# Kernel optimization log

Hardware: AMD Instinct MI355X
Metric: run time of the kernel (lower is better)

## Reference

```python
import jax, jax.numpy as jnp
import numpy as np

C_M, C_Z, C_H = 256, 128, 32
EPS = 1e-3
LN_EPS = 1e-5


def setup_inputs() -> dict:
    key = jax.random.key(0)
    ks = jax.random.split(key, 10)
    S, R = 128, 256
    inp = {
        'm_1': jax.random.normal(ks[0], (S, R, C_M), jnp.float32),
        'm_2': jax.random.normal(ks[1], (S, R, C_M), jnp.float32),
        'mask_1': jnp.ones((S, R), jnp.float32),
        'mask_2': jnp.ones((S, R), jnp.float32),
        # LayerNorm params
        'ln1_w': jnp.ones((C_M,), jnp.float32),
        'ln1_b': jnp.zeros((C_M,), jnp.float32),
        'ln2_w': jnp.ones((C_M,), jnp.float32),
        'ln2_b': jnp.zeros((C_M,), jnp.float32),
        # Linear params
        'w1': jax.random.normal(ks[2], (C_M, C_H), jnp.float32) * (1.0 / np.sqrt(C_M)),
        'b1': jnp.zeros((C_H,), jnp.float32),
        'w2': jax.random.normal(ks[3], (C_M, C_H), jnp.float32) * (1.0 / np.sqrt(C_M)),
        'b2': jnp.zeros((C_H,), jnp.float32),
        'w_out': jax.random.normal(ks[4], (C_H * C_H, C_Z), jnp.float32) * 0.02,
        'b_out': jnp.zeros((C_Z,), jnp.float32),
    }
    return inp


def _layer_norm(x, w, b):
    mu = jnp.mean(x, axis=-1, keepdims=True)
    var = jnp.mean(jnp.square(x - mu), axis=-1, keepdims=True)
    return (x - mu) * jax.lax.rsqrt(var + LN_EPS) * w + b


def reference(m_1, m_2, mask_1, mask_2, ln1_w, ln1_b, ln2_w, ln2_b,
              w1, b1, w2, b2, w_out, b_out):
    # m_*: [S, R, C_M]; mask_*: [S, R]
    a = (_layer_norm(m_1, ln1_w, ln1_b) @ w1 + b1) * mask_1[..., None]  # [S,R,H]
    b = (_layer_norm(m_2, ln2_w, ln2_b) @ w2 + b2) * mask_2[..., None]  # [S,R,H]
    # outer product mean over sequence dim: [R, R, H, H]
    outer = jnp.einsum('sic,sje->ijce', a, b)
    S, R, H = a.shape
    outer = outer.reshape(R, R, H * H)
    z = outer @ w_out + b_out  # [R, R, C_Z]
    norm = jnp.einsum('si,sj->ij', mask_1, mask_2)[..., None] + EPS  # [R,R,1]
    return z / norm
```

## Files before the change

kernel.cpp:

```cpp
#include <hip/hip_runtime.h>
#include <hip/hip_bf16.h>

#define S_DIM 128
#define R_DIM 256
#define CM    256
#define H_DIM 32
#define CZ    128

typedef short s8v   __attribute__((ext_vector_type(8)));
typedef float f32x4 __attribute__((ext_vector_type(4)));
typedef float f32x16 __attribute__((ext_vector_type(16)));
using bf16 = __hip_bfloat16;

static __device__ __forceinline__ unsigned short bf16_bits(float f) {
  return __builtin_bit_cast(unsigned short, __float2bfloat16(f));
}

static __device__ __forceinline__ void gload_lds16(const void* g, void* l) {
  __builtin_amdgcn_global_load_lds(
      (const __attribute__((address_space(1))) unsigned int*)g,
      (__attribute__((address_space(3))) unsigned int*)l, 16, 0, 0);
}

__global__ __launch_bounds__(256) void opm_prep(
    const float* __restrict__ w_out,
    const float* __restrict__ mask1, const float* __restrict__ mask2,
    const float* __restrict__ w1, const float* __restrict__ w2,
    bf16* __restrict__ wT2, float* __restrict__ rnorm, bf16* __restrict__ wF)
{
  const int b   = blockIdx.x;
  const int tid = threadIdx.x;
  if (b < 64) {
    const int vid  = b*256 + tid;
    const int lane = vid & 63;
    const int ks2  = (vid >> 6) & 63;
    const int tb   = vid >> 12;
    const int t    = tb*32 + (lane & 31);
    const int hf   = lane >> 5;
    unsigned int pk[4];
    #pragma unroll
    for (int ep = 0; ep < 4; ++ep) {
      const int ce0 = ks2*16 + hf*8 + ep*2;
      const int ce1 = ce0 + 1;
      unsigned int w0 = bf16_bits(w_out[((ce0 & 31)*32 + (ce0 >> 5))*CZ + t]);
      unsigned int w1b = bf16_bits(w_out[((ce1 & 31)*32 + (ce1 >> 5))*CZ + t]);
      pk[ep] = w0 | (w1b << 16);
    }
    uint4 o = {pk[0], pk[1], pk[2], pk[3]};
    *reinterpret_cast<uint4*>((char*)wT2 + (size_t)vid*16) = o;
  } else if (b < 320) {
    const int i = b - 64;
    const int j = tid;
    float acc = 0.f;
    for (int s = 0; s < S_DIM; ++s)
      acc += mask1[(size_t)s*R_DIM + i] * mask2[(size_t)s*R_DIM + j];
    rnorm[i*R_DIM + j] = 1.0f / (acc + 1e-3f);
  } else {
    const int mat = b - 320;
    const float* __restrict__ w = mat ? w2 : w1;
    bf16* __restrict__ dst = wF + mat*8192;
    #pragma unroll
    for (int it = 0; it < 4; ++it) {
      const int vid  = it*256 + tid;
      const int nf   = vid >> 9;
      const int ks   = (vid >> 6) & 7;
      const int lane = vid & 63;
      const int h    = nf*16 + (lane & 15);
      unsigned int pk[4];
      #pragma unroll
      for (int ep = 0; ep < 4; ++ep) {
        const int c0 = ks*32 + (lane >> 4)*8 + ep*2;
        unsigned int lo = bf16_bits(w[c0*H_DIM + h]);
        unsigned int hi = bf16_bits(w[(c0 + 1)*H_DIM + h]);
        pk[ep] = lo | (hi << 16);
      }
      uint4 o = {pk[0], pk[1], pk[2], pk[3]};
      *reinterpret_cast<uint4*>((char*)dst + (size_t)vid*16) = o;
    }
  }
}

__global__ __launch_bounds__(64) void opm_proj(
    const float* __restrict__ m1, const float* __restrict__ m2,
    const float* __restrict__ ln1w, const float* __restrict__ ln1b,
    const float* __restrict__ ln2w, const float* __restrict__ ln2b,
    const float* __restrict__ b1, const float* __restrict__ b2,
    const float* __restrict__ mask1, const float* __restrict__ mask2,
    const bf16* __restrict__ wF, bf16* __restrict__ aT, bf16* __restrict__ bT)
{
  __shared__ char xn[8192];

  const int mat = blockIdx.y;
  const float* __restrict__ m    = mat ? m2   : m1;
  const float* __restrict__ lnw  = mat ? ln2w : ln1w;
  const float* __restrict__ lnb  = mat ? ln2b : ln1b;
  const float* __restrict__ bias = mat ? b2   : b1;
  const float* __restrict__ mask = mat ? mask2 : mask1;
  const bf16* __restrict__ wf    = wF + mat*8192;
  bf16* __restrict__ dst         = mat ? bT   : aT;

  const int lane = threadIdx.x;
  const int row  = lane & 15;
  const int q    = lane >> 4;
  const int r    = blockIdx.x & 255;
  const int sb   = blockIdx.x >> 8;
  const int s    = sb*16 + row;

  const float4* __restrict__ src =
      reinterpret_cast<const float4*>(m + ((size_t)s*R_DIM + r)*CM + q*64);
  float4 x[16];
  float sum = 0.f, sq = 0.f;
  #pragma unroll
  for (int i = 0; i < 16; ++i) {
    x[i] = src[i];
    sum += x[i].x + x[i].y + x[i].z + x[i].w;
    sq  += x[i].x*x[i].x + x[i].y*x[i].y + x[i].z*x[i].z + x[i].w*x[i].w;
  }
  sum += __shfl_xor(sum, 16); sum += __shfl_xor(sum, 32);
  sq  += __shfl_xor(sq, 16);  sq  += __shfl_xor(sq, 32);
  const float mu = sum * (1.0f/CM);
  const float rs = rsqrtf(sq * (1.0f/CM) - mu*mu + 1e-5f);

  const float4* __restrict__ lw4 = reinterpret_cast<const float4*>(lnw + q*64);
  const float4* __restrict__ lb4 = reinterpret_cast<const float4*>(lnb + q*64);
  #pragma unroll
  for (int i2 = 0; i2 < 8; ++i2) {
    unsigned int pk[4];
    #pragma unroll
    for (int half = 0; half < 2; ++half) {
      const int i = i2*2 + half;
      const float4 lw = lw4[i];
      const float4 lb = lb4[i];
      const float v0 = (x[i].x - mu)*rs*lw.x + lb.x;
      const float v1 = (x[i].y - mu)*rs*lw.y + lb.y;
      const float v2 = (x[i].z - mu)*rs*lw.z + lb.z;
      const float v3 = (x[i].w - mu)*rs*lw.w + lb.w;
      pk[half*2+0] = (unsigned)bf16_bits(v0) | ((unsigned)bf16_bits(v1) << 16);
      pk[half*2+1] = (unsigned)bf16_bits(v2) | ((unsigned)bf16_bits(v3) << 16);
    }
    int off = row*512 + q*128 + i2*16;
    off ^= (row & 7) << 4;
    uint4 o = {pk[0], pk[1], pk[2], pk[3]};
    *reinterpret_cast<uint4*>(xn + off) = o;
  }
  __syncthreads();

  const float bv0 = bias[row];
  const float bv1 = bias[16 + row];
  f32x4 z0 = {bv0, bv0, bv0, bv0};
  f32x4 z1 = {bv1, bv1, bv1, bv1};
  #pragma unroll
  for (int ks = 0; ks < 8; ++ks) {
    int off = row*512 + ks*64 + q*16;
    off ^= (row & 7) << 4;
    const s8v a  = *reinterpret_cast<const s8v*>(xn + off);
    const s8v w0 = *reinterpret_cast<const s8v*>((const char*)wf + (ks*64 + lane)*16);
    const s8v w1 = *reinterpret_cast<const s8v*>((const char*)wf + ((8 + ks)*64 + lane)*16);
    z0 = __builtin_amdgcn_mfma_f32_16x16x32_bf16(a, w0, z0, 0, 0, 0);
    z1 = __builtin_amdgcn_mfma_f32_16x16x32_bf16(a, w1, z1, 0, 0, 0);
  }

  float mk[4];
  #pragma unroll
  for (int rr = 0; rr < 4; ++rr)
    mk[rr] = mask[(size_t)(sb*16 + q*4 + rr)*R_DIM + r];

  unsigned int pa0 = (unsigned)bf16_bits(z0[0]*mk[0]) | ((unsigned)bf16_bits(z0[1]*mk[1]) << 16);
  unsigned int pa1 = (unsigned)bf16_bits(z0[2]*mk[2]) | ((unsigned)bf16_bits(z0[3]*mk[3]) << 16);
  unsigned int pb0 = (unsigned)bf16_bits(z1[0]*mk[0]) | ((unsigned)bf16_bits(z1[1]*mk[1]) << 16);
  unsigned int pb1 = (unsigned)bf16_bits(z1[2]*mk[2]) | ((unsigned)bf16_bits(z1[3]*mk[3]) << 16);

  const int p0 = r*H_DIM + row;
  const int p1 = r*H_DIM + 16 + row;
  const int c0 = sb*2 + (q >> 1);
  const int rem = (q & 1) * 8;
  {
    uint2 v; v.x = pa0; v.y = pa1;
    *reinterpret_cast<uint2*>((char*)dst + (size_t)p0*256 + ((c0 ^ (p0 & 15)) << 4) + rem) = v;
  }
  {
    uint2 v; v.x = pb0; v.y = pb1;
    *reinterpret_cast<uint2*>((char*)dst + (size_t)p1*256 + ((c0 ^ (p1 & 15)) << 4) + rem) = v;
  }
}

__global__ __launch_bounds__(1024, 4) void opm_gemm(
    const bf16* __restrict__ aT, const bf16* __restrict__ bT,
    const bf16* __restrict__ wT2, const float* __restrict__ b_out,
    const float* __restrict__ rnorm, float* __restrict__ out)
{
  __shared__ char smem[131072];

  const int tid  = threadIdx.x;
  const int lane = tid & 63;
  const int wid  = tid >> 6;
  const int l31  = lane & 31;
  const int hf   = lane >> 5;

  int swz = blockIdx.x;
  swz = (swz & 7)*128 + (swz >> 3);
  const int bx = swz >> 5, by = swz & 31;

  {
    const char* gA = (const char*)aT + (size_t)bx*65536;
    const char* gB = (const char*)bT + (size_t)by*65536;
    #pragma unroll
    for (int i = 0; i < 4; ++i) {
      const int base = (i*16 + wid)*1024;
      gload_lds16(gA + base + lane*16, smem + base);
      gload_lds16(gB + base + lane*16, smem + 65536 + base);
    }
  }
  __syncthreads();

  const int wm = wid >> 2, wn = wid & 3;
  f32x16 acc[2][2];
  #pragma unroll
  for (int mf = 0; mf < 2; ++mf)
    #pragma unroll
    for (int nf = 0; nf < 2; ++nf)
      #pragma unroll
      for (int r = 0; r < 16; ++r) acc[mf][nf][r] = 0.f;

  #pragma unroll
  for (int ks = 0; ks < 8; ++ks) {
    s8v af[2], bfv[2];
    #pragma unroll
    for (int mf = 0; mf < 2; ++mf) {
      const int mm = wm*64 + mf*32 + l31;
      int L = (mm*256 + ks*32 + hf*16) ^ ((mm & 15) << 4);
      af[mf] = *reinterpret_cast<const s8v*>(smem + L);
    }
    #pragma unroll
    for (int nf = 0; nf < 2; ++nf) {
      const int nn = wn*64 + nf*32 + l31;
      int L = (nn*256 + ks*32 + hf*16) ^ ((nn & 15) << 4);
      bfv[nf] = *reinterpret_cast<const s8v*>(smem + 65536 + L);
    }
    #pragma unroll
    for (int mf = 0; mf < 2; ++mf)
      #pragma unroll
      for (int nf = 0; nf < 2; ++nf)
        acc[mf][nf] = __builtin_amdgcn_mfma_f32_32x32x16_bf16(af[mf], bfv[nf], acc[mf][nf], 0, 0, 0);
  }
  __syncthreads();

  const int kq = wm, pn = wn;
  const char* wb = (const char*)wT2 + ((size_t)(pn*64 + kq*16)*64 + lane)*16;
  s8v bwr[16];

  #pragma unroll
  for (int i = 0; i < 8; ++i)
    bwr[i] = *reinterpret_cast<const s8v*>(wb + i*1024);

  #pragma unroll
  for (int nf = 0; nf < 2; ++nf) {
    const int pair = (wm*2 + 0)*8 + wn*2 + nf;
    #pragma unroll
    for (int g = 0; g < 4; ++g) {
      const unsigned int lo = (unsigned)bf16_bits(acc[0][nf][4*g+0]) |
                              ((unsigned)bf16_bits(acc[0][nf][4*g+1]) << 16);
      const unsigned int hi = (unsigned)bf16_bits(acc[0][nf][4*g+2]) |
                              ((unsigned)bf16_bits(acc[0][nf][4*g+3]) << 16);
      const int L0 = pair*2048 + (l31*32 + 8*g + 4*hf)*2;
      const int L  = L0 ^ ((((pair & 15) ^ ((L0 >> 7) & 15))) << 4);
      uint2 v; v.x = lo; v.y = hi;
      *reinterpret_cast<uint2*>(smem + L) = v;
    }
  }

  #pragma unroll
  for (int i = 8; i < 16; ++i)
    bwr[i] = *reinterpret_cast<const s8v*>(wb + i*1024);

  #pragma unroll
  for (int nf = 0; nf < 2; ++nf) {
    const int pair = (wm*2 + 1)*8 + wn*2 + nf;
    #pragma unroll
    for (int g = 0; g < 4; ++g) {
      const unsigned int lo = (unsigned)bf16_bits(acc[1][nf][4*g+0]) |
                              ((unsigned)bf16_bits(acc[1][nf][4*g+1]) << 16);
      const unsigned int hi = (unsigned)bf16_bits(acc[1][nf][4*g+2]) |
                              ((unsigned)bf16_bits(acc[1][nf][4*g+3]) << 16);
      const int L0 = pair*2048 + (l31*32 + 8*g + 4*hf)*2;
      const int L  = L0 ^ ((((pair & 15) ^ ((L0 >> 7) & 15))) << 4);
      uint2 v; v.x = lo; v.y = hi;
      *reinterpret_cast<uint2*>(smem + L) = v;
    }
  }
  __syncthreads();

  const int t = pn*32 + l31;
  f32x16 z0, z1;
  {
    const float init = (kq == 0) ? b_out[t] : 0.f;
    #pragma unroll
    for (int r = 0; r < 16; ++r) { z0[r] = init; z1[r] = init; }
  }
  #pragma unroll
  for (int ks = 0; ks < 16; ++ks) {
    const int ks2 = kq*16 + ks;
    {
      const int pair = l31;
      int L0 = pair*2048 + ks2*32 + hf*16;
      int L  = L0 ^ ((((pair & 15) ^ ((L0 >> 7) & 15))) << 4);
      const s8v a = *reinterpret_cast<const s8v*>(smem + L);
      z0 = __builtin_amdgcn_mfma_f32_32x32x16_bf16(a, bwr[ks], z0, 0, 0, 0);
    }
    {
      const int pair = 32 + l31;
      int L0 = pair*2048 + ks2*32 + hf*16;
      int L  = L0 ^ ((((pair & 15) ^ ((L0 >> 7) & 15))) << 4);
      const s8v a = *reinterpret_cast<const s8v*>(smem + L);
      z1 = __builtin_amdgcn_mfma_f32_32x32x16_bf16(a, bwr[ks], z1, 0, 0, 0);
    }
  }
  __syncthreads();

  {
    const int base = wid*8192;
    #pragma unroll
    for (int g = 0; g < 4; ++g) {
      f32x4 v0 = {z0[4*g+0], z0[4*g+1], z0[4*g+2], z0[4*g+3]};
      f32x4 v1 = {z1[4*g+0], z1[4*g+1], z1[4*g+2], z1[4*g+3]};
      *reinterpret_cast<f32x4*>(smem + base +        g*1024 + lane*16) = v0;
      *reinterpret_cast<f32x4*>(smem + base + 4096 + g*1024 + lane*16) = v1;
    }
  }
  __syncthreads();

  {
    const int chain = kq & 1;
    const int gh    = kq >> 1;
    f32x4 f[2];
    #pragma unroll
    for (int gg = 0; gg < 2; ++gg) {
      const int g = gh*2 + gg;
      f32x4 s = {0.f, 0.f, 0.f, 0.f};
      #pragma unroll
      for (int kk = 0; kk < 4; ++kk) {
        const int base = (kk*4 + pn)*8192 + chain*4096;
        const f32x4 p = *reinterpret_cast<const f32x4*>(smem + base + g*1024 + lane*16);
        #pragma unroll
        for (int j = 0; j < 4; ++j) s[j] += p[j];
      }
      f[gg] = s;
    }
    #pragma unroll
    for (int gg = 0; gg < 2; ++gg) {
      const int g = gh*2 + gg;
      #pragma unroll
      for (int j = 0; j < 4; ++j) {
        const int row  = j + 4*hf + 8*g;
        const int pair = chain*32 + row;
        const int o    = (bx*8 + (pair >> 3))*R_DIM + by*8 + (pair & 7);
        out[(size_t)o*CZ + t] = f[gg][j] * rnorm[o];
      }
    }
  }
}

extern "C" void kernel_launch(void* const* d_in, const int* in_sizes, int n_in,
                              void* d_out, int out_size, void* d_ws, size_t ws_size,
                              hipStream_t stream) {
  const float* m_1    = (const float*)d_in[0];
  const float* m_2    = (const float*)d_in[1];
  const float* mask_1 = (const float*)d_in[2];
  const float* mask_2 = (const float*)d_in[3];
  const float* ln1_w  = (const float*)d_in[4];
  const float* ln1_b  = (const float*)d_in[5];
  const float* ln2_w  = (const float*)d_in[6];
  const float* ln2_b  = (const float*)d_in[7];
  const float* w1     = (const float*)d_in[8];
  const float* b1     = (const float*)d_in[9];
  const float* w2     = (const float*)d_in[10];
  const float* b2     = (const float*)d_in[11];
  const float* w_out  = (const float*)d_in[12];
  const float* b_out  = (const float*)d_in[13];
  float* out = (float*)d_out;

  char* ws = (char*)d_ws;
  bf16* aT    = (bf16*)ws;
  bf16* bT    = (bf16*)(ws + (2u << 20));
  bf16* wT2   = (bf16*)(ws + (4u << 20));
  float* rnrm = (float*)(ws + (4u << 20) + (256u << 10));
  bf16* wF    = (bf16*)(ws + (4u << 20) + (512u << 10));

  opm_prep<<<dim3(322),      dim3(256), 0, stream>>>(w_out, mask_1, mask_2,
      w1, w2, wT2, rnrm, wF);
  opm_proj<<<dim3(2048, 2),  dim3(64),  0, stream>>>(m_1, m_2, ln1_w, ln1_b,
      ln2_w, ln2_b, b1, b2, mask_1, mask_2, wF, aT, bT);
  opm_gemm<<<dim3(1024),     dim3(1024), 0, stream>>>(aT, bT, wT2, b_out, rnrm, out);
}
```

Baseline: 77.13 us.

## Make GEMM blocks loop over four B tiles with register prefetch of next tile

The grid shrinks from 1024 to 256 workgroups. Each workgroup now computes four consecutive by tiles in a loop instead of one, keeps the A tile resident, and prefetches the next B tile (and an A reload) into registers during the epilogue before writing it to LDS. The goal is to hide global-load latency and cut launch and tail overhead per output tile. In exchange it loses parallelism: 256 blocks of 1024 threads may underfill the GPU, and the extra syncs and serial loop add latency.

Measured after the change: 185.0 us. 2.4x slower.

```diff
diff --git a/kernel.cpp b/kernel.cpp
--- a/kernel.cpp
+++ b/kernel.cpp
@@ -197,165 +197,195 @@
   const int l31  = lane & 31;
   const int hf   = lane >> 5;
 
-  int swz = blockIdx.x;
-  swz = (swz & 7)*128 + (swz >> 3);
-  const int bx = swz >> 5, by = swz & 31;
+  const int wg  = blockIdx.x;
+  const int swz = (wg & 7)*32 + (wg >> 3);
+  const int bx  = swz >> 3;
+  const int g   = swz & 7;
+
+  const int wm = wid >> 2, wn = wid & 3;
+  const int kq = wm, pn = wn;
+
+  const char* gA = (const char*)aT + (size_t)bx*65536;
 
   {
-    const char* gA = (const char*)aT + (size_t)bx*65536;
-    const char* gB = (const char*)bT + (size_t)by*65536;
+    const char* gB = (const char*)bT + (size_t)(g*4)*65536;
     #pragma unroll
     for (int i = 0; i < 4; ++i) {
-      const int base = (i*16 + wid)*1024;
-      gload_lds16(gA + base + lane*16, smem + base);
-      gload_lds16(gB + base + lane*16, smem + 65536 + base);
+      const int base = (i*16 + wid)*1024 + lane*16;
+      gload_lds16(gA + base, smem + base);
+      gload_lds16(gB + base, smem + 65536 + base);
     }
   }
   __syncthreads();
 
-  const int wm = wid >> 2, wn = wid & 3;
-  f32x16 acc[2][2];
-  #pragma unroll
-  for (int mf = 0; mf < 2; ++mf)
-    #pragma unroll
-    for (int nf = 0; nf < 2; ++nf)
-      #pragma unroll
-      for (int r = 0; r < 16; ++r) acc[mf][nf][r] = 0.f;
-
-  #pragma unroll
-  for (int ks = 0; ks < 8; ++ks) {
-    s8v af[2], bfv[2];
-    #pragma unroll
-    for (int mf = 0; mf < 2; ++mf) {
-      const int mm = wm*64 + mf*32 + l31;
-      int L = (mm*256 + ks*32 + hf*16) ^ ((mm & 15) << 4);
-      af[mf] = *reinterpret_cast<const s8v*>(smem + L);
-    }
+  uint4 pf[8];
+
+  #pragma unroll 1
+  for (int t = 0; t < 4; ++t) {
+    const int by = g*4 + t;
+
+    f32x16 acc[2][2];
+    #pragma unroll
+    for (int mf = 0; mf < 2; ++mf)
+      #pragma unroll
+      for (int nf = 0; nf < 2; ++nf)
+        #pragma unroll
+        for (int r = 0; r < 16; ++r) acc[mf][nf][r] = 0.f;
+
+    #pragma unroll
+    for (int ks = 0; ks < 8; ++ks) {
+      s8v af[2], bfv[2];
+      #pragma unroll
+      for (int mf = 0; mf < 2; ++mf) {
+        const int mm = wm*64 + mf*32 + l31;
+        int L = (mm*256 + ks*32 + hf*16) ^ ((mm & 15) << 4);
+        af[mf] = *reinterpret_cast<const s8v*>(smem + L);
+      }
+      #pragma unroll
+      for (int nf = 0; nf < 2; ++nf) {
+        const int nn = wn*64 + nf*32 + l31;
+        int L = (nn*256 + ks*32 + hf*16) ^ ((nn & 15) << 4);
+        bfv[nf] = *reinterpret_cast<const s8v*>(smem + 65536 + L);
+      }
+      #pragma unroll
+      for (int mf = 0; mf < 2; ++mf)
+        #pragma unroll
+        for (int nf = 0; nf < 2; ++nf)
+          acc[mf][nf] = __builtin_amdgcn_mfma_f32_32x32x16_bf16(af[mf], bfv[nf], acc[mf][nf], 0, 0, 0);
+    }
+    __syncthreads();
+
+    const char* wb = (const char*)wT2 + ((size_t)(pn*64 + kq*16)*64 + lane)*16;
+    s8v bwr[16];
+
+    #pragma unroll
+    for (int i = 0; i < 8; ++i)
+      bwr[i] = *reinterpret_cast<const s8v*>(wb + i*1024);
+
     #pragma unroll
     for (int nf = 0; nf < 2; ++nf) {
-      const int nn = wn*64 + nf*32 + l31;
-      int L = (nn*256 + ks*32 + hf*16) ^ ((nn & 15) << 4);
-      bfv[nf] = *reinterpret_cast<const s8v*>(smem + 65536 + L);
-    }
-    #pragma unroll
-    for (int mf = 0; mf < 2; ++mf)
-      #pragma unroll
-      for (int nf = 0; nf < 2; ++nf)
-        acc[mf][nf] = __builtin_amdgcn_mfma_f32_32x32x16_bf16(af[mf], bfv[nf], acc[mf][nf], 0, 0, 0);
-  }
-  __syncthreads();
-
-  const int kq = wm, pn = wn;
-  const char* wb = (const char*)wT2 + ((size_t)(pn*64 + kq*16)*64 + lane)*16;
-  s8v bwr[16];
-
-  #pragma unroll
-  for (int i = 0; i < 8; ++i)
-    bwr[i] = *reinterpret_cast<const s8v*>(wb + i*1024);
-
-  #pragma unroll
-  for (int nf = 0; nf < 2; ++nf) {
-    const int pair = (wm*2 + 0)*8 + wn*2 + nf;
-    #pragma unroll
-    for (int g = 0; g < 4; ++g) {
-      const unsigned int lo = (unsigned)bf16_bits(acc[0][nf][4*g+0]) |
-                              ((unsigned)bf16_bits(acc[0][nf][4*g+1]) << 16);
-      const unsigned int hi = (unsigned)bf16_bits(acc[0][nf][4*g+2]) |
-                              ((unsigned)bf16_bits(acc[0][nf][4*g+3]) << 16);
-      const int L0 = pair*2048 + (l31*32 + 8*g + 4*hf)*2;
-      const int L  = L0 ^ ((((pair & 15) ^ ((L0 >> 7) & 15))) << 4);
-      uint2 v; v.x = lo; v.y = hi;
-      *reinterpret_cast<uint2*>(smem + L) = v;
-    }
-  }
-
-  #pragma unroll
-  for (int i = 8; i < 16; ++i)
-    bwr[i] = *reinterpret_cast<const s8v*>(wb + i*1024);
-
-  #pragma unroll
-  for (int nf = 0; nf < 2; ++nf) {
-    const int pair = (wm*2 + 1)*8 + wn*2 + nf;
-    #pragma unroll
-    for (int g = 0; g < 4; ++g) {
-      const unsigned int lo = (unsigned)bf16_bits(acc[1][nf][4*g+0]) |
-                              ((unsigned)bf16_bits(acc[1][nf][4*g+1]) << 16);
-      const unsigned int hi = (unsigned)bf16_bits(acc[1][nf][4*g+2]) |
-                              ((unsigned)bf16_bits(acc[1][nf][4*g+3]) << 16);
-      const int L0 = pair*2048 + (l31*32 + 8*g + 4*hf)*2;
-      const int L  = L0 ^ ((((pair & 15) ^ ((L0 >> 7) & 15))) << 4);
-      uint2 v; v.x = lo; v.y = hi;
-      *reinterpret_cast<uint2*>(smem + L) = v;
-    }
-  }
-  __syncthreads();
-
-  const int t = pn*32 + l31;
-  f32x16 z0, z1;
-  {
-    const float init = (kq == 0) ? b_out[t] : 0.f;
-    #pragma unroll
-    for (int r = 0; r < 16; ++r) { z0[r] = init; z1[r] = init; }
-  }
-  #pragma unroll
-  for (int ks = 0; ks < 16; ++ks) {
-    const int ks2 = kq*16 + ks;
+      const int pair = (wm*2 + 0)*8 + wn*2 + nf;
+      #pragma unroll
+      for (int gg = 0; gg < 4; ++gg) {
+        const unsigned int lo = (unsigned)bf16_bits(acc[0][nf][4*gg+0]) |
+                                ((unsigned)bf16_bits(acc[0][nf][4*gg+1]) << 16);
+        const unsigned int hi = (unsigned)bf16_bits(acc[0][nf][4*gg+2]) |
+                                ((unsigned)bf16_bits(acc[0][nf][4*gg+3]) << 16);
+        const int L0 = pair*2048 + (l31*32 + 8*gg + 4*hf)*2;
+        const int L  = L0 ^ ((((pair & 15) ^ ((L0 >> 7) & 15))) << 4);
+        uint2 v; v.x = lo; v.y = hi;
+        *reinterpret_cast<uint2*>(smem + L) = v;
+      }
+    }
+
+    #pragma unroll
+    for (int i = 8; i < 16; ++i)
+      bwr[i] = *reinterpret_cast<const s8v*>(wb + i*1024);
+
+    #pragma unroll
+    for (int nf = 0; nf < 2; ++nf) {
+      const int pair = (wm*2 + 1)*8 + wn*2 + nf;
+      #pragma unroll
+      for (int gg = 0; gg < 4; ++gg) {
+        const unsigned int lo = (unsigned)bf16_bits(acc[1][nf][4*gg+0]) |
+                                ((unsigned)bf16_bits(acc[1][nf][4*gg+1]) << 16);
+        const unsigned int hi = (unsigned)bf16_bits(acc[1][nf][4*gg+2]) |
+                                ((unsigned)bf16_bits(acc[1][nf][4*gg+3]) << 16);
+        const int L0 = pair*2048 + (l31*32 + 8*gg + 4*hf)*2;
+        const int L  = L0 ^ ((((pair & 15) ^ ((L0 >> 7) & 15))) << 4);
+        uint2 v; v.x = lo; v.y = hi;
+        *reinterpret_cast<uint2*>(smem + L) = v;
+      }
+    }
+    __syncthreads();
+
+    const int tcol = pn*32 + l31;
+    f32x16 z0, z1;
     {
-      const int pair = l31;
-      int L0 = pair*2048 + ks2*32 + hf*16;
-      int L  = L0 ^ ((((pair & 15) ^ ((L0 >> 7) & 15))) << 4);
-      const s8v a = *reinterpret_cast<const s8v*>(smem + L);
-      z0 = __builtin_amdgcn_mfma_f32_32x32x16_bf16(a, bwr[ks], z0, 0, 0, 0);
-    }
+      const float init = (kq == 0) ? b_out[tcol] : 0.f;
+      #pragma unroll
+      for (int r = 0; r < 16; ++r) { z0[r] = init; z1[r] = init; }
+    }
+    #pragma unroll
+    for (int ks = 0; ks < 16; ++ks) {
+      const int ks2 = kq*16 + ks;
+      {
+        const int pair = l31;
+        int L0 = pair*2048 + ks2*32 + hf*16;
+        int L  = L0 ^ ((((pair & 15) ^ ((L0 >> 7) & 15))) << 4);
+        const s8v a = *reinterpret_cast<const s8v*>(smem + L);
+        z0 = __builtin_amdgcn_mfma_f32_32x32x16_bf16(a, bwr[ks], z0, 0, 0, 0);
+      }
+      {
+        const int pair = 32 + l31;
+        int L0 = pair*2048 + ks2*32 + hf*16;
+        int L  = L0 ^ ((((pair & 15) ^ ((L0 >> 7) & 15))) << 4);
+        const s8v a = *reinterpret_cast<const s8v*>(smem + L);
+        z1 = __builtin_amdgcn_mfma_f32_32x32x16_bf16(a, bwr[ks], z1, 0, 0, 0);
+      }
+    }
+    __syncthreads();
+
     {
-      const int pair = 32 + l31;
-      int L0 = pair*2048 + ks2*32 + hf*16;
-      int L  = L0 ^ ((((pair & 15) ^ ((L0 >> 7) & 15))) << 4);
-      const s8v a = *reinterpret_cast<const s8v*>(smem + L);
-      z1 = __builtin_amdgcn_mfma_f32_32x32x16_bf16(a, bwr[ks], z1, 0, 0, 0);
-    }
-  }
-  __syncthreads();
-
-  {
-    const int base = wid*8192;
-    #pragma unroll
-    for (int g = 0; g < 4; ++g) {
-      f32x4 v0 = {z0[4*g+0], z0[4*g+1], z0[4*g+2], z0[4*g+3]};
-      f32x4 v1 = {z1[4*g+0], z1[4*g+1], z1[4*g+2], z1[4*g+3]};
-      *reinterpret_cast<f32x4*>(smem + base +        g*1024 + lane*16) = v0;
-      *reinterpret_cast<f32x4*>(smem + base + 4096 + g*1024 + lane*16) = v1;
-    }
-  }
-  __syncthreads();
-
-  {
-    const int chain = kq & 1;
-    const int gh    = kq >> 1;
-    f32x4 f[2];
-    #pragma unroll
-    for (int gg = 0; gg < 2; ++gg) {
-      const int g = gh*2 + gg;
-      f32x4 s = {0.f, 0.f, 0.f, 0.f};
-      #pragma unroll
-      for (int kk = 0; kk < 4; ++kk) {
-        const int base = (kk*4 + pn)*8192 + chain*4096;
-        const f32x4 p = *reinterpret_cast<const f32x4*>(smem + base + g*1024 + lane*16);
+      const int base = wid*8192;
+      #pragma unroll
+      for (int gg = 0; gg < 4; ++gg) {
+        f32x4 v0 = {z0[4*gg+0], z0[4*gg+1], z0[4*gg+2], z0[4*gg+3]};
+        f32x4 v1 = {z1[4*gg+0], z1[4*gg+1], z1[4*gg+2], z1[4*gg+3]};
+        *reinterpret_cast<f32x4*>(smem + base +        gg*1024 + lane*16) = v0;
+        *reinterpret_cast<f32x4*>(smem + base + 4096 + gg*1024 + lane*16) = v1;
+      }
+    }
+    if (t < 3) {
+      const char* gB = (const char*)bT + (size_t)(by + 1)*65536;
+      #pragma unroll
+      for (int c = 0; c < 4; ++c) {
+        const int L = (c*16 + wid)*1024 + lane*16;
+        pf[c]     = *reinterpret_cast<const uint4*>(gA + L);
+        pf[c + 4] = *reinterpret_cast<const uint4*>(gB + L);
+      }
+    }
+    __syncthreads();
+
+    {
+      const int chain = kq & 1;
+      const int gh    = kq >> 1;
+      f32x4 f[2];
+      #pragma unroll
+      for (int gg = 0; gg < 2; ++gg) {
+        const int gidx = gh*2 + gg;
+        f32x4 s = {0.f, 0.f, 0.f, 0.f};
         #pragma unroll
-        for (int j = 0; j < 4; ++j) s[j] += p[j];
-      }
-      f[gg] = s;
-    }
-    #pragma unroll
-    for (int gg = 0; gg < 2; ++gg) {
-      const int g = gh*2 + gg;
-      #pragma unroll
-      for (int j = 0; j < 4; ++j) {
-        const int row  = j + 4*hf + 8*g;
-        const int pair = chain*32 + row;
-        const int o    = (bx*8 + (pair >> 3))*R_DIM + by*8 + (pair & 7);
-        out[(size_t)o*CZ + t] = f[gg][j] * rnorm[o];
-      }
+        for (int kk = 0; kk < 4; ++kk) {
+          const int base = (kk*4 + pn)*8192 + chain*4096;
+          const f32x4 p = *reinterpret_cast<const f32x4*>(smem + base + gidx*1024 + lane*16);
+          #pragma unroll
+          for (int j = 0; j < 4; ++j) s[j] += p[j];
+        }
+        f[gg] = s;
+      }
+      #pragma unroll
+      for (int gg = 0; gg < 2; ++gg) {
+        const int gidx = gh*2 + gg;
+        #pragma unroll
+        for (int j = 0; j < 4; ++j) {
+          const int row  = j + 4*hf + 8*gidx;
+          const int pair = chain*32 + row;
+          const int o    = (bx*8 + (pair >> 3))*R_DIM + by*8 + (pair & 7);
+          out[(size_t)o*CZ + tcol] = f[gg][j] * rnorm[o];
+        }
+      }
+    }
+
+    if (t < 3) {
+      __syncthreads();
+      #pragma unroll
+      for (int c = 0; c < 4; ++c) {
+        const int L = (c*16 + wid)*1024 + lane*16;
+        *reinterpret_cast<uint4*>(smem + L)         = pf[c];
+        *reinterpret_cast<uint4*>(smem + 65536 + L) = pf[c + 4];
+      }
+      __syncthreads();
     }
   }
 }
@@ -390,5 +420,5 @@
       w1, w2, wT2, rnrm, wF);
   opm_proj<<<dim3(2048, 2),  dim3(64),  0, stream>>>(m_1, m_2, ln1_w, ln1_b,
       ln2_w, ln2_b, b1, b2, mask_1, mask_2, wF, aT, bT);
-  opm_gemm<<<dim3(1024),     dim3(1024), 0, stream>>>(aT, bT, wT2, b_out, rnrm, out);
-}
+  opm_gemm<<<dim3(256),      dim3(1024), 0, stream>>>(aT, bT, wT2, b_out, rnrm, out);
+}
```
